# Kernel optimization log

Measured on AMD Instinct MI355X. Metric: run time of the kernel, lower is better.

Reference implementation:

```python
import jax, jax.numpy as jnp
import numpy as np

B, S, H, HD = 8, 1024, 16, 64
D = H * HD
NINF = -10000.0
EPS = 1e-6


def setup_inputs() -> dict:
    key = jax.random.key(0)
    ks = jax.random.split(key, 6)
    std = 0.02
    return {
        "x": jax.random.normal(ks[0], (B, S, D), jnp.float32),
        "mask": jax.random.randint(ks[1], (B, S), 0, 2, jnp.int32),
        "wq": jax.random.normal(ks[2], (D, D), jnp.float32) * std,
        "bq": jnp.zeros((D,), jnp.float32),
        "wk": jax.random.normal(ks[3], (D, D), jnp.float32) * std,
        "bk": jnp.zeros((D,), jnp.float32),
        "wv": jax.random.normal(ks[4], (D, D), jnp.float32) * std,
        "bv": jnp.zeros((D,), jnp.float32),
        "wo": jax.random.normal(ks[5], (D, D), jnp.float32) * std,
        "bo": jnp.zeros((D,), jnp.float32),
        "gamma": jnp.ones((D,), jnp.float32),
        "beta": jnp.zeros((D,), jnp.float32),
    }


def _heads(t):
    # [B,S,D] -> [B,H,S,HD]
    return t.reshape(t.shape[0], t.shape[1], H, HD).transpose(0, 2, 1, 3)


def _layernorm(x, gamma, beta):
    mu = jnp.mean(x, -1, keepdims=True)
    var = jnp.mean(jnp.square(x - mu), -1, keepdims=True)
    return (x - mu) * jax.lax.rsqrt(var + EPS) * gamma + beta


def reference(x, mask, wq, bq, wk, bk, wv, bv, wo, bo, gamma, beta):
    q = _heads(x @ wq + bq)
    k = _heads(x @ wk + bk)
    v = _heads(x @ wv + bv)
    scores = jnp.einsum("bhqd,bhkd->bhqk", q, k) / np.sqrt(HD).astype(np.float32)
    # padding mask broadcast over key axis: 1 = masked
    scores = scores + mask.astype(jnp.float32)[:, None, None, :] * NINF
    attn = jax.nn.softmax(scores, axis=-1)
    ctx = jnp.einsum("bhqk,bhkd->bhqd", attn, v)  # [B,H,S,HD]
    ctx = ctx.transpose(0, 2, 1, 3).reshape(B, S, D)
    out = _layernorm(x + ctx @ wo + bo, gamma, beta)
    return out
```

## Files before the change

kernel.cpp:

```cpp
#include <hip/hip_runtime.h>
#include <stdint.h>

typedef unsigned short u16;
typedef unsigned int u32;
typedef __bf16 b16x8 __attribute__((ext_vector_type(8)));
typedef float f32x4 __attribute__((ext_vector_type(4)));

#define B_ 8
#define S_ 1024
#define H_ 16
#define HD_ 64
#define D_ 1024
#define M_ 8192

__device__ __forceinline__ u16 f2bf(float f) {
  u32 u = __float_as_uint(f);
  return (u16)((u + 0x7fffu + ((u >> 16) & 1u)) >> 16);
}

__device__ __forceinline__ f32x4 mfma16(b16x8 a, b16x8 b, f32x4 c) {
  return __builtin_amdgcn_mfma_f32_16x16x32_bf16(a, b, c, 0, 0, 0);
}

__device__ __forceinline__ void cp16(const u16* g, u16* l) {
  __builtin_amdgcn_global_load_lds(
      (const __attribute__((address_space(1))) u32*)(g),
      (__attribute__((address_space(3))) u32*)(l), 16, 0, 0);
}

__global__ __launch_bounds__(1024) void wconv_kernel(
    const float* __restrict__ w0, const float* __restrict__ w1,
    const float* __restrict__ w2, const float* __restrict__ w3,
    u16* __restrict__ t0, u16* __restrict__ t1, u16* __restrict__ t2,
    u16* __restrict__ t3) {
  __shared__ float tile[32][33];
  const int z = blockIdx.z;
  const float* src = (z == 0) ? w0 : (z == 1) ? w1 : (z == 2) ? w2 : w3;
  u16* dst = (z == 0) ? t0 : (z == 1) ? t1 : (z == 2) ? t2 : t3;
  const int tx = threadIdx.x, ty = threadIdx.y;
  const int x0 = blockIdx.x * 32, y0 = blockIdx.y * 32;
  tile[ty][tx] = src[(size_t)(y0 + ty) * D_ + x0 + tx];
  __syncthreads();
  dst[(size_t)(x0 + ty) * D_ + y0 + tx] = f2bf(tile[tx][ty]);
}

__global__ __launch_bounds__(256) void xconv_kernel(const float* __restrict__ x,
                                                    u16* __restrict__ xb) {
  const size_t i = ((size_t)blockIdx.x * 256 + threadIdx.x) * 4;
  const float4 v = *(const float4*)(x + i);
  u16 o[4] = {f2bf(v.x), f2bf(v.y), f2bf(v.z), f2bf(v.w)};
  uint2 pack;
  pack.x = ((u32)o[1] << 16) | o[0];
  pack.y = ((u32)o[3] << 16) | o[2];
  *(uint2*)(xb + i) = pack;
}

__device__ __forceinline__ void gemm128_mainloop(
    const u16* __restrict__ A, const u16* __restrict__ BT, int K, int m0,
    int n0, u16* lds, f32x4 (&acc)[4][4]) {
  const int t = threadIdx.x;
  const int lane = t & 63;
  const int w = t >> 6;
  const int l15 = lane & 15;
  const int q4 = lane >> 4;
  const int mwave = (w >> 1) * 64;
  const int nwave = (w & 1) * 64;

  u16* Alds = lds;
  u16* Blds = lds + 4096;

  const f32x4 zero = {0.f, 0.f, 0.f, 0.f};
  for (int mt = 0; mt < 4; ++mt)
    for (int nt = 0; nt < 4; ++nt) acc[mt][nt] = zero;

  const int srow = t >> 2;
  const int scol = (t & 3) * 8;
  const u16* Ag = A + (size_t)(m0 + srow) * K + scol;
  const u16* Bg = BT + (size_t)(n0 + srow) * K + scol;
  u16* Al = Alds + t * 8;
  u16* Bl = Blds + t * 8;

  for (int k0 = 0; k0 < K; k0 += 32) {
    __syncthreads();
    cp16(Ag + k0, Al);
    cp16(Ag + (size_t)64 * K + k0, Al + 2048);
    cp16(Bg + k0, Bl);
    cp16(Bg + (size_t)64 * K + k0, Bl + 2048);
    __syncthreads();

    b16x8 af[4], bf[4];
    for (int mt = 0; mt < 4; ++mt)
      af[mt] = *(const b16x8*)(Alds + (mwave + mt * 16 + l15) * 32 + q4 * 8);
    for (int nt = 0; nt < 4; ++nt)
      bf[nt] = *(const b16x8*)(Blds + (nwave + nt * 16 + l15) * 32 + q4 * 8);
    for (int mt = 0; mt < 4; ++mt)
      for (int nt = 0; nt < 4; ++nt)
        acc[mt][nt] = mfma16(af[mt], bf[nt], acc[mt][nt]);
  }
}

__global__ __launch_bounds__(256) void qkv_gemm_kernel(
    const u16* __restrict__ xb, const u16* __restrict__ wtq,
    const u16* __restrict__ wtk, const u16* __restrict__ wtv,
    const float* __restrict__ bq, const float* __restrict__ bk,
    const float* __restrict__ bv, u16* __restrict__ Q, u16* __restrict__ Kb,
    u16* __restrict__ VT) {
  __shared__ __align__(16) u16 lds[8192];
  const int z = blockIdx.z;
  const u16* BTp = (z == 0) ? wtq : (z == 1) ? wtk : wtv;
  const float* bias = (z == 0) ? bq : (z == 1) ? bk : bv;
  u16* out = (z == 0) ? Q : (z == 1) ? Kb : VT;
  const int m0 = blockIdx.y * 128, n0 = blockIdx.x * 128;

  f32x4 acc[4][4];
  gemm128_mainloop(xb, BTp, D_, m0, n0, lds, acc);

  const int lane = threadIdx.x & 63, w = threadIdx.x >> 6;
  const int l15 = lane & 15, q4 = lane >> 4;
  const int mwave = (w >> 1) * 64, nwave = (w & 1) * 64;

  for (int nt = 0; nt < 4; ++nt) {
    const int n = n0 + nwave + nt * 16 + l15;
    const float bias_v = bias[n];
    const int h = n >> 6, hd = n & 63;
    for (int mt = 0; mt < 4; ++mt) {
      for (int r = 0; r < 4; ++r) {
        const int m = m0 + mwave + mt * 16 + q4 * 4 + r;
        const int b = m >> 10, s = m & 1023;
        const float v = acc[mt][nt][r] + bias_v;
        size_t idx;
        if (z < 2)
          idx = (((size_t)(b * H_ + h)) * S_ + s) * HD_ + hd;
        else
          idx = (((size_t)(b * H_ + h)) * HD_ + hd) * S_ + s;
        out[idx] = f2bf(v);
      }
    }
  }
}

#define PAD_ 72
__global__ __launch_bounds__(256) void attn_kernel(
    const u16* __restrict__ Q, const u16* __restrict__ Kb,
    const u16* __restrict__ VT, const int* __restrict__ mask,
    u16* __restrict__ ctx) {
  __shared__ __align__(16) u16 Qlds[64 * PAD_];
  __shared__ __align__(16) u16 Klds[64 * PAD_];
  __shared__ __align__(16) u16 Vlds[64 * PAD_];
  __shared__ __align__(16) u16 Plds[4][16 * PAD_];

  const int t = threadIdx.x;
  const int lane = t & 63, w = t >> 6;
  const int l15 = lane & 15, q4 = lane >> 4;
  const int bh = blockIdx.y;
  const int b = bh >> 4, h = bh & 15;
  const int q0 = blockIdx.x * 64;

  const u16* Qbh = Q + (size_t)bh * S_ * HD_;
  const u16* Kbh = Kb + (size_t)bh * S_ * HD_;
  const u16* Vbh = VT + (size_t)bh * S_ * HD_;
  const int* maskb = mask + b * S_;

  const int srow = t >> 3, scol = (t & 7) * 8;
  {
    b16x8 q0v = *(const b16x8*)(Qbh + (size_t)(q0 + srow) * HD_ + scol);
    b16x8 q1v = *(const b16x8*)(Qbh + (size_t)(q0 + srow + 32) * HD_ + scol);
    *(b16x8*)(Qlds + srow * PAD_ + scol) = q0v;
    *(b16x8*)(Qlds + (srow + 32) * PAD_ + scol) = q1v;
  }
  __syncthreads();
  b16x8 aq[2];
  aq[0] = *(const b16x8*)(Qlds + (w * 16 + l15) * PAD_ + q4 * 8);
  aq[1] = *(const b16x8*)(Qlds + (w * 16 + l15) * PAD_ + 32 + q4 * 8);

  const f32x4 zero = {0.f, 0.f, 0.f, 0.f};
  f32x4 acc[4];
  for (int nt = 0; nt < 4; ++nt) acc[nt] = zero;
  float lsum[4] = {0.f, 0.f, 0.f, 0.f};
  u16* Pw = Plds[w];
  const float c1 = 0.18033688f;

  for (int j = 0; j < 16; ++j) {
    const int key0 = j * 64;
    b16x8 k0v = *(const b16x8*)(Kbh + (size_t)(key0 + srow) * HD_ + scol);
    b16x8 k1v = *(const b16x8*)(Kbh + (size_t)(key0 + srow + 32) * HD_ + scol);
    b16x8 v0v = *(const b16x8*)(Vbh + (size_t)srow * S_ + key0 + scol);
    b16x8 v1v = *(const b16x8*)(Vbh + (size_t)(srow + 32) * S_ + key0 + scol);
    float madd[4];
    for (int nt = 0; nt < 4; ++nt)
      madd[nt] = -14427.0f * (float)maskb[key0 + nt * 16 + l15];
    __syncthreads();
    *(b16x8*)(Klds + srow * PAD_ + scol) = k0v;
    *(b16x8*)(Klds + (srow + 32) * PAD_ + scol) = k1v;
    *(b16x8*)(Vlds + srow * PAD_ + scol) = v0v;
    *(b16x8*)(Vlds + (srow + 32) * PAD_ + scol) = v1v;
    __syncthreads();

    f32x4 sf[4];
    for (int nt = 0; nt < 4; ++nt) sf[nt] = zero;
    for (int kk = 0; kk < 2; ++kk)
      for (int nt = 0; nt < 4; ++nt) {
        b16x8 bk =
            *(const b16x8*)(Klds + (nt * 16 + l15) * PAD_ + kk * 32 + q4 * 8);
        sf[nt] = mfma16(aq[kk], bk, sf[nt]);
      }

    float p[4][4];
    for (int nt = 0; nt < 4; ++nt)
      for (int r = 0; r < 4; ++r) {
        p[nt][r] = __builtin_amdgcn_exp2f(sf[nt][r] * c1 + madd[nt]);
        lsum[r] += p[nt][r];
      }

    for (int nt = 0; nt < 4; ++nt)
      for (int r = 0; r < 4; ++r)
        Pw[(q4 * 4 + r) * PAD_ + nt * 16 + l15] = f2bf(p[nt][r]);
    __syncthreads();

    for (int kk = 0; kk < 2; ++kk) {
      b16x8 ap = *(const b16x8*)(Pw + l15 * PAD_ + kk * 32 + q4 * 8);
      for (int nt = 0; nt < 4; ++nt) {
        b16x8 vb =
            *(const b16x8*)(Vlds + (nt * 16 + l15) * PAD_ + kk * 32 + q4 * 8);
        acc[nt] = mfma16(ap, vb, acc[nt]);
      }
    }
  }

  for (int r = 0; r < 4; ++r)
    for (int off = 1; off < 16; off <<= 1) lsum[r] += __shfl_xor(lsum[r], off);

  for (int nt = 0; nt < 4; ++nt) {
    const int dcol = h * 64 + nt * 16 + l15;
    for (int r = 0; r < 4; ++r) {
      const int srw = q0 + w * 16 + q4 * 4 + r;
      const float o = acc[nt][r] / lsum[r];
      ctx[((size_t)(b * S_ + srw)) * D_ + dcol] = f2bf(o);
    }
  }
}

__global__ __launch_bounds__(256) void out_gemm_kernel(
    const u16* __restrict__ ctx, const u16* __restrict__ wto,
    const float* __restrict__ bo, const float* __restrict__ x,
    float* __restrict__ y) {
  __shared__ __align__(16) u16 lds[8192];
  const int m0 = blockIdx.y * 128, n0 = blockIdx.x * 128;
  f32x4 acc[4][4];
  gemm128_mainloop(ctx, wto, D_, m0, n0, lds, acc);

  const int lane = threadIdx.x & 63, w = threadIdx.x >> 6;
  const int l15 = lane & 15, q4 = lane >> 4;
  const int mwave = (w >> 1) * 64, nwave = (w & 1) * 64;

  for (int nt = 0; nt < 4; ++nt) {
    const int n = n0 + nwave + nt * 16 + l15;
    const float bias = bo[n];
    for (int mt = 0; mt < 4; ++mt) {
      for (int r = 0; r < 4; ++r) {
        const int m = m0 + mwave + mt * 16 + q4 * 4 + r;
        y[(size_t)m * D_ + n] = acc[mt][nt][r] + bias + x[(size_t)m * D_ + n];
      }
    }
  }
}

__global__ __launch_bounds__(256) void ln_kernel(const float* __restrict__ y,
                                                 const float* __restrict__ g,
                                                 const float* __restrict__ be,
                                                 float* __restrict__ out) {
  const int row = blockIdx.x, t = threadIdx.x;
  const float* yr = y + (size_t)row * D_;
  const float4 v = *(const float4*)(yr + t * 4);
  float s = v.x + v.y + v.z + v.w;
  float ss = v.x * v.x + v.y * v.y + v.z * v.z + v.w * v.w;
  for (int off = 1; off < 64; off <<= 1) {
    s += __shfl_xor(s, off);
    ss += __shfl_xor(ss, off);
  }
  __shared__ float red[8];
  const int w = t >> 6, lane = t & 63;
  if (lane == 0) {
    red[w] = s;
    red[4 + w] = ss;
  }
  __syncthreads();
  s = red[0] + red[1] + red[2] + red[3];
  ss = red[4] + red[5] + red[6] + red[7];
  const float mu = s * (1.f / 1024.f);
  const float var = ss * (1.f / 1024.f) - mu * mu;
  const float rs = rsqrtf(var + 1e-6f);
  const int c = t * 4;
  const float4 gv = *(const float4*)(g + c);
  const float4 bv = *(const float4*)(be + c);
  float4 o;
  o.x = (v.x - mu) * rs * gv.x + bv.x;
  o.y = (v.y - mu) * rs * gv.y + bv.y;
  o.z = (v.z - mu) * rs * gv.z + bv.z;
  o.w = (v.w - mu) * rs * gv.w + bv.w;
  *(float4*)(out + (size_t)row * D_ + c) = o;
}

extern "C" void kernel_launch(void* const* d_in, const int* in_sizes, int n_in,
                              void* d_out, int out_size, void* d_ws,
                              size_t ws_size, hipStream_t stream) {
  const float* x = (const float*)d_in[0];
  const int* mask = (const int*)d_in[1];
  const float* wq = (const float*)d_in[2];
  const float* bq = (const float*)d_in[3];
  const float* wk = (const float*)d_in[4];
  const float* bk = (const float*)d_in[5];
  const float* wv = (const float*)d_in[6];
  const float* bv = (const float*)d_in[7];
  const float* wo = (const float*)d_in[8];
  const float* bo = (const float*)d_in[9];
  const float* gamma = (const float*)d_in[10];
  const float* beta = (const float*)d_in[11];
  float* out = (float*)d_out;

  char* ws = (char*)d_ws;
  const size_t MB = 1024ull * 1024ull;
  u16* wtq = (u16*)(ws + 0 * MB);
  u16* wtk = (u16*)(ws + 2 * MB);
  u16* wtv = (u16*)(ws + 4 * MB);
  u16* wto = (u16*)(ws + 6 * MB);
  u16* xb = (u16*)(ws + 8 * MB);
  u16* ctx = (u16*)(ws + 8 * MB);
  u16* Qb = (u16*)(ws + 24 * MB);
  u16* Kb = (u16*)(ws + 40 * MB);
  u16* VTb = (u16*)(ws + 56 * MB);
  float* y = (float*)(ws + 24 * MB);

  wconv_kernel<<<dim3(32, 32, 4), dim3(32, 32), 0, stream>>>(
      wq, wk, wv, wo, wtq, wtk, wtv, wto);
  xconv_kernel<<<8192, 256, 0, stream>>>(x, xb);
  qkv_gemm_kernel<<<dim3(8, 64, 3), 256, 0, stream>>>(
      xb, wtq, wtk, wtv, bq, bk, bv, Qb, Kb, VTb);
  attn_kernel<<<dim3(16, 128), 256, 0, stream>>>(Qb, Kb, VTb, mask, ctx);
  out_gemm_kernel<<<dim3(8, 64), 256, 0, stream>>>(ctx, wto, bo, x, y);
  ln_kernel<<<8192, 256, 0, stream>>>(y, gamma, beta, out);
}
```

Before: 317.7 us.

## Widen GEMM K-tile with swizzled LDS and double attention query tile

The shared GEMM mainloop now stages 64-wide K slices per iteration. It uses an XOR-swizzled LDS layout to avoid bank conflicts and halve the number of barriers. The attention kernel processes 128 queries per block, two MFMA row fragments per wave, so each K/V tile loaded into LDS is reused twice. It also replaces the block barrier after writing the per-wave P tile with an LDS waitcnt and changes padding to 68. The tradeoffs are more registers and LDS per block. The PAD of 68 also makes 16-byte LDS accesses only 8-byte aligned, which may split or slow those accesses.

```diff
diff --git a/kernel.cpp b/kernel.cpp
--- a/kernel.cpp
+++ b/kernel.cpp
@@ -67,35 +67,45 @@
   const int nwave = (w & 1) * 64;
 
   u16* Alds = lds;
-  u16* Blds = lds + 4096;
+  u16* Blds = lds + 8192;
 
   const f32x4 zero = {0.f, 0.f, 0.f, 0.f};
   for (int mt = 0; mt < 4; ++mt)
     for (int nt = 0; nt < 4; ++nt) acc[mt][nt] = zero;
 
-  const int srow = t >> 2;
-  const int scol = (t & 3) * 8;
-  const u16* Ag = A + (size_t)(m0 + srow) * K + scol;
-  const u16* Bg = BT + (size_t)(n0 + srow) * K + scol;
-  u16* Al = Alds + t * 8;
-  u16* Bl = Blds + t * 8;
-
-  for (int k0 = 0; k0 < K; k0 += 32) {
+  const int rbase = t >> 3;
+  const int scol = ((t & 7) ^ (rbase & 7)) * 8;
+  const u16* Ag = A + (size_t)(m0 + rbase) * K + scol;
+  const u16* Bg = BT + (size_t)(n0 + rbase) * K + scol;
+
+  const int sx = l15 & 7;
+  const int cA0 = ((0 * 4 + q4) ^ sx) * 8;
+  const int cA1 = ((1 * 4 + q4) ^ sx) * 8;
+
+  for (int k0 = 0; k0 < K; k0 += 64) {
     __syncthreads();
-    cp16(Ag + k0, Al);
-    cp16(Ag + (size_t)64 * K + k0, Al + 2048);
-    cp16(Bg + k0, Bl);
-    cp16(Bg + (size_t)64 * K + k0, Bl + 2048);
+    for (int c = 0; c < 4; ++c) {
+      cp16(Ag + (size_t)(c * 32) * K + k0, Alds + c * 2048 + t * 8);
+      cp16(Bg + (size_t)(c * 32) * K + k0, Blds + c * 2048 + t * 8);
+    }
     __syncthreads();
 
-    b16x8 af[4], bf[4];
+    b16x8 af[4][2], bfr[4][2];
+    for (int mt = 0; mt < 4; ++mt) {
+      const int row = (mwave + mt * 16 + l15) * 64;
+      af[mt][0] = *(const b16x8*)(Alds + row + cA0);
+      af[mt][1] = *(const b16x8*)(Alds + row + cA1);
+    }
+    for (int nt = 0; nt < 4; ++nt) {
+      const int row = (nwave + nt * 16 + l15) * 64;
+      bfr[nt][0] = *(const b16x8*)(Blds + row + cA0);
+      bfr[nt][1] = *(const b16x8*)(Blds + row + cA1);
+    }
     for (int mt = 0; mt < 4; ++mt)
-      af[mt] = *(const b16x8*)(Alds + (mwave + mt * 16 + l15) * 32 + q4 * 8);
-    for (int nt = 0; nt < 4; ++nt)
-      bf[nt] = *(const b16x8*)(Blds + (nwave + nt * 16 + l15) * 32 + q4 * 8);
-    for (int mt = 0; mt < 4; ++mt)
-      for (int nt = 0; nt < 4; ++nt)
-        acc[mt][nt] = mfma16(af[mt], bf[nt], acc[mt][nt]);
+      for (int nt = 0; nt < 4; ++nt) {
+        acc[mt][nt] = mfma16(af[mt][0], bfr[nt][0], acc[mt][nt]);
+        acc[mt][nt] = mfma16(af[mt][1], bfr[nt][1], acc[mt][nt]);
+      }
   }
 }
 
@@ -105,7 +115,7 @@
     const float* __restrict__ bq, const float* __restrict__ bk,
     const float* __restrict__ bv, u16* __restrict__ Q, u16* __restrict__ Kb,
     u16* __restrict__ VT) {
-  __shared__ __align__(16) u16 lds[8192];
+  __shared__ __align__(16) u16 lds[16384];
   const int z = blockIdx.z;
   const u16* BTp = (z == 0) ? wtq : (z == 1) ? wtk : wtv;
   const float* bias = (z == 0) ? bq : (z == 1) ? bk : bv;
@@ -139,22 +149,22 @@
   }
 }
 
-#define PAD_ 72
+#define PAD_ 68
 __global__ __launch_bounds__(256) void attn_kernel(
     const u16* __restrict__ Q, const u16* __restrict__ Kb,
     const u16* __restrict__ VT, const int* __restrict__ mask,
     u16* __restrict__ ctx) {
-  __shared__ __align__(16) u16 Qlds[64 * PAD_];
+  __shared__ __align__(16) u16 Qlds[128 * PAD_];
   __shared__ __align__(16) u16 Klds[64 * PAD_];
   __shared__ __align__(16) u16 Vlds[64 * PAD_];
-  __shared__ __align__(16) u16 Plds[4][16 * PAD_];
+  __shared__ __align__(16) u16 Plds[4][32 * PAD_];
 
   const int t = threadIdx.x;
   const int lane = t & 63, w = t >> 6;
   const int l15 = lane & 15, q4 = lane >> 4;
   const int bh = blockIdx.y;
   const int b = bh >> 4, h = bh & 15;
-  const int q0 = blockIdx.x * 64;
+  const int q0 = blockIdx.x * 128;
 
   const u16* Qbh = Q + (size_t)bh * S_ * HD_;
   const u16* Kbh = Kb + (size_t)bh * S_ * HD_;
@@ -163,20 +173,24 @@
 
   const int srow = t >> 3, scol = (t & 7) * 8;
   {
-    b16x8 q0v = *(const b16x8*)(Qbh + (size_t)(q0 + srow) * HD_ + scol);
-    b16x8 q1v = *(const b16x8*)(Qbh + (size_t)(q0 + srow + 32) * HD_ + scol);
-    *(b16x8*)(Qlds + srow * PAD_ + scol) = q0v;
-    *(b16x8*)(Qlds + (srow + 32) * PAD_ + scol) = q1v;
+    for (int g = 0; g < 4; ++g) {
+      b16x8 qv =
+          *(const b16x8*)(Qbh + (size_t)(q0 + srow + g * 32) * HD_ + scol);
+      *(b16x8*)(Qlds + (srow + g * 32) * PAD_ + scol) = qv;
+    }
   }
   __syncthreads();
-  b16x8 aq[2];
-  aq[0] = *(const b16x8*)(Qlds + (w * 16 + l15) * PAD_ + q4 * 8);
-  aq[1] = *(const b16x8*)(Qlds + (w * 16 + l15) * PAD_ + 32 + q4 * 8);
+  b16x8 aq[2][2];
+  for (int mf = 0; mf < 2; ++mf)
+    for (int kk = 0; kk < 2; ++kk)
+      aq[mf][kk] = *(const b16x8*)(Qlds + (w * 32 + mf * 16 + l15) * PAD_ +
+                                   kk * 32 + q4 * 8);
 
   const f32x4 zero = {0.f, 0.f, 0.f, 0.f};
-  f32x4 acc[4];
-  for (int nt = 0; nt < 4; ++nt) acc[nt] = zero;
-  float lsum[4] = {0.f, 0.f, 0.f, 0.f};
+  f32x4 acc[2][4];
+  for (int mf = 0; mf < 2; ++mf)
+    for (int nt = 0; nt < 4; ++nt) acc[mf][nt] = zero;
+  float lsum[2][4] = {{0.f, 0.f, 0.f, 0.f}, {0.f, 0.f, 0.f, 0.f}};
   u16* Pw = Plds[w];
   const float c1 = 0.18033688f;
 
@@ -196,55 +210,61 @@
     *(b16x8*)(Vlds + (srow + 32) * PAD_ + scol) = v1v;
     __syncthreads();
 
-    f32x4 sf[4];
-    for (int nt = 0; nt < 4; ++nt) sf[nt] = zero;
+    f32x4 sf[2][4];
+    for (int mf = 0; mf < 2; ++mf)
+      for (int nt = 0; nt < 4; ++nt) sf[mf][nt] = zero;
     for (int kk = 0; kk < 2; ++kk)
       for (int nt = 0; nt < 4; ++nt) {
         b16x8 bk =
             *(const b16x8*)(Klds + (nt * 16 + l15) * PAD_ + kk * 32 + q4 * 8);
-        sf[nt] = mfma16(aq[kk], bk, sf[nt]);
-      }
-
-    float p[4][4];
-    for (int nt = 0; nt < 4; ++nt)
-      for (int r = 0; r < 4; ++r) {
-        p[nt][r] = __builtin_amdgcn_exp2f(sf[nt][r] * c1 + madd[nt]);
-        lsum[r] += p[nt][r];
-      }
-
-    for (int nt = 0; nt < 4; ++nt)
-      for (int r = 0; r < 4; ++r)
-        Pw[(q4 * 4 + r) * PAD_ + nt * 16 + l15] = f2bf(p[nt][r]);
-    __syncthreads();
+        for (int mf = 0; mf < 2; ++mf)
+          sf[mf][nt] = mfma16(aq[mf][kk], bk, sf[mf][nt]);
+      }
+
+    for (int mf = 0; mf < 2; ++mf)
+      for (int nt = 0; nt < 4; ++nt)
+        for (int r = 0; r < 4; ++r) {
+          const float p = __builtin_amdgcn_exp2f(sf[mf][nt][r] * c1 + madd[nt]);
+          lsum[mf][r] += p;
+          Pw[(mf * 16 + q4 * 4 + r) * PAD_ + nt * 16 + l15] = f2bf(p);
+        }
+    asm volatile("s_waitcnt lgkmcnt(0)" ::: "memory");
 
     for (int kk = 0; kk < 2; ++kk) {
-      b16x8 ap = *(const b16x8*)(Pw + l15 * PAD_ + kk * 32 + q4 * 8);
+      b16x8 ap[2];
+      for (int mf = 0; mf < 2; ++mf)
+        ap[mf] =
+            *(const b16x8*)(Pw + (mf * 16 + l15) * PAD_ + kk * 32 + q4 * 8);
       for (int nt = 0; nt < 4; ++nt) {
         b16x8 vb =
             *(const b16x8*)(Vlds + (nt * 16 + l15) * PAD_ + kk * 32 + q4 * 8);
-        acc[nt] = mfma16(ap, vb, acc[nt]);
-      }
-    }
-  }
-
-  for (int r = 0; r < 4; ++r)
-    for (int off = 1; off < 16; off <<= 1) lsum[r] += __shfl_xor(lsum[r], off);
-
-  for (int nt = 0; nt < 4; ++nt) {
-    const int dcol = h * 64 + nt * 16 + l15;
-    for (int r = 0; r < 4; ++r) {
-      const int srw = q0 + w * 16 + q4 * 4 + r;
-      const float o = acc[nt][r] / lsum[r];
-      ctx[((size_t)(b * S_ + srw)) * D_ + dcol] = f2bf(o);
-    }
-  }
+        for (int mf = 0; mf < 2; ++mf)
+          acc[mf][nt] = mfma16(ap[mf], vb, acc[mf][nt]);
+      }
+    }
+  }
+
+  for (int mf = 0; mf < 2; ++mf)
+    for (int r = 0; r < 4; ++r)
+      for (int off = 1; off < 16; off <<= 1)
+        lsum[mf][r] += __shfl_xor(lsum[mf][r], off);
+
+  for (int mf = 0; mf < 2; ++mf)
+    for (int nt = 0; nt < 4; ++nt) {
+      const int dcol = h * 64 + nt * 16 + l15;
+      for (int r = 0; r < 4; ++r) {
+        const int srw = q0 + w * 32 + mf * 16 + q4 * 4 + r;
+        const float o = acc[mf][nt][r] / lsum[mf][r];
+        ctx[((size_t)(b * S_ + srw)) * D_ + dcol] = f2bf(o);
+      }
+    }
 }
 
 __global__ __launch_bounds__(256) void out_gemm_kernel(
     const u16* __restrict__ ctx, const u16* __restrict__ wto,
     const float* __restrict__ bo, const float* __restrict__ x,
     float* __restrict__ y) {
-  __shared__ __align__(16) u16 lds[8192];
+  __shared__ __align__(16) u16 lds[16384];
   const int m0 = blockIdx.y * 128, n0 = blockIdx.x * 128;
   f32x4 acc[4][4];
   gemm128_mainloop(ctx, wto, D_, m0, n0, lds, acc);
@@ -336,7 +356,7 @@
   xconv_kernel<<<8192, 256, 0, stream>>>(x, xb);
   qkv_gemm_kernel<<<dim3(8, 64, 3), 256, 0, stream>>>(
       xb, wtq, wtk, wtv, bq, bk, bv, Qb, Kb, VTb);
-  attn_kernel<<<dim3(16, 128), 256, 0, stream>>>(Qb, Kb, VTb, mask, ctx);
+  attn_kernel<<<dim3(8, 128), 256, 0, stream>>>(Qb, Kb, VTb, mask, ctx);
   out_gemm_kernel<<<dim3(8, 64), 256, 0, stream>>>(ctx, wto, bo, x, y);
   ln_kernel<<<8192, 256, 0, stream>>>(y, gamma, beta, out);
 }
```

Result: slower. 338.2 us (+6.4%).
